# Kernel optimization log

Measured on AMD Instinct MI355X. Metric: run time of the kernel, lower is better.

The kernel has to match this reference:

```python
import jax, jax.numpy as jnp
import numpy as np

B, M = 4, 8192
NUM_PAD = 1024  # trailing pc columns zeroed to exercise the zero-column mask


def setup_inputs() -> dict:
    key = jax.random.key(0)
    k1, k2 = jax.random.split(key)
    vertices = jax.random.normal(k1, (B, 3, 128, 64), dtype=jnp.float32)
    pc = jax.random.normal(k2, (B, 3, M), dtype=jnp.float32)
    # zero-pad some columns: the original filters columns where all 3 coords == 0
    pc = pc.at[:, :, M - NUM_PAD:].set(0.0)
    return {"vertices": vertices, "pc": pc}


def reference(vertices, pc):
    b = vertices.shape[0]
    v = vertices.reshape(b, 3, -1).transpose(0, 2, 1)   # [B, N, 3] mesh vertices
    p = pc.transpose(0, 2, 1)                           # [B, M, 3] point cloud
    valid = ~jnp.all(pc == 0.0, axis=1)                 # [B, M] non-zero columns
    # squared pairwise distances pc -> vertices: [B, M, N]
    d2 = (
        jnp.sum(p * p, axis=-1)[:, :, None]
        + jnp.sum(v * v, axis=-1)[:, None, :]
        - 2.0 * jnp.einsum("bmd,bnd->bmn", p, v)
    )
    dist2 = jnp.min(d2, axis=-1)                        # [B, M] NN sq-dist per pc point
    valid_f = valid.astype(dist2.dtype)
    per_item = jnp.sum(dist2 * valid_f, axis=-1) / jnp.sum(valid_f, axis=-1)  # mean over valid points
    return jnp.mean(per_item)
```

## Files before the change

### kernel.cpp

```cpp
#include <hip/hip_runtime.h>

typedef float v2f __attribute__((ext_vector_type(2)));

#define MPTS 8192
#define NVERT 8192
#define TPB 256
#define PPT 8
#define BQ (TPB*PPT)
#define NCHUNK 32
#define VC (NVERT/NCHUNK)
#define VPAIRS (VC/2)

__global__ __launch_bounds__(TPB, 2) void minpart_kernel(
        const float* __restrict__ vert,
        const float* __restrict__ pc,
        float* __restrict__ partial)
{
    __shared__ float4 lvA[VPAIRS];
    __shared__ float4 lvB[VPAIRS];
    const int b = blockIdx.z, chunk = blockIdx.y;
    const int mbase = blockIdx.x * BQ;
    const int tid = threadIdx.x;

    const float* vb = vert + (size_t)b * 3 * NVERT + chunk * VC;
    if (tid < VPAIRS) {
        const v2f x = ((const v2f*)vb)[tid];
        const v2f y = ((const v2f*)(vb + NVERT))[tid];
        const v2f z = ((const v2f*)(vb + 2 * NVERT))[tid];
        const v2f w = x * x + y * y + z * z;
        lvA[tid] = make_float4(x.x, x.y, y.x, y.y);
        lvB[tid] = make_float4(z.x, z.y, w.x, w.y);
    }

    const float* pcb = pc + (size_t)b * 3 * MPTS;
    v2f npx[PPT], npy[PPT], npz[PPT], acc[PPT];
    #pragma unroll
    for (int p = 0; p < PPT; ++p) {
        const int m = mbase + p * TPB + tid;
        const float x = pcb[m], y = pcb[MPTS + m], z = pcb[2 * MPTS + m];
        npx[p] = (v2f){-2.0f * x, -2.0f * x};
        npy[p] = (v2f){-2.0f * y, -2.0f * y};
        npz[p] = (v2f){-2.0f * z, -2.0f * z};
        acc[p] = (v2f){1e30f, 1e30f};
    }
    __syncthreads();

    #pragma unroll 2
    for (int j = 0; j < VPAIRS; ++j) {
        const float4 A = lvA[j], Bv = lvB[j];
        const v2f vx = {A.x, A.y}, vy = {A.z, A.w};
        const v2f vz = {Bv.x, Bv.y}, vw = {Bv.z, Bv.w};
        #pragma unroll
        for (int p = 0; p < PPT; ++p) {
            const v2f t = __builtin_elementwise_fma(npx[p], vx,
                           __builtin_elementwise_fma(npy[p], vy,
                            __builtin_elementwise_fma(npz[p], vz, vw)));
            acc[p] = __builtin_elementwise_min(acc[p], t);
        }
    }

    float* po = partial + ((size_t)b * NCHUNK + chunk) * MPTS + mbase + tid;
    #pragma unroll
    for (int p = 0; p < PPT; ++p)
        po[p * TPB] = fminf(acc[p].x, acc[p].y);
}

__global__ __launch_bounds__(64) void reduce_kernel(
        const float* __restrict__ pc,
        const float* __restrict__ partial,
        v2f* __restrict__ part)
{
    const int b = blockIdx.x >> 5, sl = blockIdx.x & 31;
    const int tid = threadIdx.x;
    const int m = sl * 256 + tid * 4;
    const float* pcb = pc + (size_t)b * 3 * MPTS;
    const float* pb  = partial + (size_t)b * NCHUNK * MPTS;

    float4 t = *(const float4*)(pb + m);
    #pragma unroll 8
    for (int c = 1; c < NCHUNK; ++c) {
        const float4 u = *(const float4*)(pb + (size_t)c * MPTS + m);
        t.x = fminf(t.x, u.x); t.y = fminf(t.y, u.y);
        t.z = fminf(t.z, u.z); t.w = fminf(t.w, u.w);
    }
    const float4 x = *(const float4*)(pcb + m);
    const float4 y = *(const float4*)(pcb + MPTS + m);
    const float4 z = *(const float4*)(pcb + 2 * MPTS + m);

    float sum = 0.0f, cnt = 0.0f;
    {
        const float xs[4] = {x.x, x.y, x.z, x.w};
        const float ys[4] = {y.x, y.y, y.z, y.w};
        const float zs[4] = {z.x, z.y, z.z, z.w};
        const float ts[4] = {t.x, t.y, t.z, t.w};
        #pragma unroll
        for (int i = 0; i < 4; ++i) {
            const float d2 = fmaf(xs[i], xs[i], fmaf(ys[i], ys[i],
                             fmaf(zs[i], zs[i], ts[i])));
            if (!(xs[i] == 0.0f && ys[i] == 0.0f && zs[i] == 0.0f)) {
                sum += d2; cnt += 1.0f;
            }
        }
    }
    #pragma unroll
    for (int off = 32; off; off >>= 1) {
        sum += __shfl_down(sum, off);
        cnt += __shfl_down(cnt, off);
    }
    if (tid == 0) part[blockIdx.x] = (v2f){sum, cnt};
}

__global__ __launch_bounds__(128) void final_kernel(
        const v2f* __restrict__ part, float* __restrict__ out, int B)
{
    __shared__ float ss[128], sc[128];
    const int t = threadIdx.x;
    v2f p = (v2f){0.0f, 0.0f};
    if (t < B * 32) p = part[t];
    ss[t] = p.x; sc[t] = p.y;
    __syncthreads();
    if (t == 0) {
        float acc = 0.0f;
        for (int b = 0; b < B; ++b) {
            float s = 0.0f, c = 0.0f;
            for (int i = 0; i < 32; ++i) { s += ss[b * 32 + i]; c += sc[b * 32 + i]; }
            acc += s / c;
        }
        out[0] = acc / (float)B;
    }
}

extern "C" void kernel_launch(void* const* d_in, const int* in_sizes, int n_in,
                              void* d_out, int out_size, void* d_ws, size_t ws_size,
                              hipStream_t stream) {
    const float* vert = (const float*)d_in[0];
    const float* pc   = (const float*)d_in[1];
    float* out        = (float*)d_out;
    const int B = in_sizes[0] / (3 * NVERT);

    float* partial = (float*)d_ws;
    v2f* part = (v2f*)(partial + (size_t)B * NCHUNK * MPTS);

    dim3 grid(MPTS / BQ, NCHUNK, B);
    minpart_kernel<<<grid, TPB, 0, stream>>>(vert, pc, partial);
    reduce_kernel<<<B * 32, 64, 0, stream>>>(pc, partial, part);
    final_kernel<<<1, 128, 0, stream>>>(part, out, B);
}
```

Baseline: 83.56 us.

## Compute distance tiles with bf16x3 split MFMA instead of FP32 FMA loops

Moves the inner pairwise-distance computation onto 32x32x16 bf16 MFMA instructions. Each float operand is split into high and low bf16 parts so the dot product, plus the |v|^2 term, keeps near-FP32 accuracy. A new prep kernel packs vertex fragments into an MFMA-ready layout, and the vertex-chunk split drops from 32 to 2, which shrinks the partial-min traffic. The risks are reduced precision in the minimum distance from the truncated bf16 split and the added cost of an extra prep launch.

```diff
diff --git a/kernel.cpp b/kernel.cpp
--- a/kernel.cpp
+++ b/kernel.cpp
@@ -1,68 +1,108 @@
 #include <hip/hip_runtime.h>
 
-typedef float v2f __attribute__((ext_vector_type(2)));
+typedef float v2f    __attribute__((ext_vector_type(2)));
+typedef float f32x16 __attribute__((ext_vector_type(16)));
+typedef short short8 __attribute__((ext_vector_type(8)));
 
 #define MPTS 8192
 #define NVERT 8192
+#define NTILE (NVERT/32)
+#define NCHUNK 2
 #define TPB 256
-#define PPT 8
-#define BQ (TPB*PPT)
-#define NCHUNK 32
-#define VC (NVERT/NCHUNK)
-#define VPAIRS (VC/2)
+
+static __device__ __forceinline__ unsigned short bhi(float f) {
+    return (unsigned short)(__float_as_uint(f) >> 16);
+}
+static __device__ __forceinline__ float bf2f(unsigned short h) {
+    return __uint_as_float(((unsigned int)h) << 16);
+}
+
+__global__ __launch_bounds__(TPB) void prep_kernel(
+        const float* __restrict__ vert,
+        unsigned short* __restrict__ bfrag)
+{
+    const int idx = blockIdx.x * TPB + threadIdx.x;
+    const int b = idx >> 13, v = idx & (NVERT - 1);
+    const float* vb = vert + (size_t)b * 3 * NVERT;
+    const float x = vb[v], y = vb[v + NVERT], z = vb[v + 2 * NVERT];
+    const unsigned short hx = bhi(x), hy = bhi(y), hz = bhi(z);
+    const unsigned short lx = bhi(x - bf2f(hx));
+    const unsigned short ly = bhi(y - bf2f(hy));
+    const unsigned short lz = bhi(z - bf2f(hz));
+    const float w = fmaf(x, x, fmaf(y, y, z * z));
+    const unsigned short hw = bhi(w);
+    const unsigned short lw = bhi(w - bf2f(hw));
+
+    const int tile = v >> 5, c = v & 31;
+    unsigned short* base = bfrag + ((size_t)b * NTILE + tile) * 512;
+    short8 g0 = {(short)hx, (short)hy, (short)hz,
+                 (short)hx, (short)hy, (short)hz, (short)lx, (short)ly};
+    short8 g1 = {(short)lz, (short)hw, (short)lw, 0, 0, 0, 0, 0};
+    *(short8*)(base + c * 8)        = g0;
+    *(short8*)(base + (c + 32) * 8) = g1;
+}
 
 __global__ __launch_bounds__(TPB, 2) void minpart_kernel(
-        const float* __restrict__ vert,
+        const unsigned short* __restrict__ bfrag,
         const float* __restrict__ pc,
         float* __restrict__ partial)
 {
-    __shared__ float4 lvA[VPAIRS];
-    __shared__ float4 lvB[VPAIRS];
     const int b = blockIdx.z, chunk = blockIdx.y;
-    const int mbase = blockIdx.x * BQ;
     const int tid = threadIdx.x;
+    const int wave = tid >> 6, l = tid & 63;
+    const int half = l >> 5, lm = l & 31;
+    const int strip = blockIdx.x * 4 + wave;
+    const int pm = strip * 32 + lm;
 
-    const float* vb = vert + (size_t)b * 3 * NVERT + chunk * VC;
-    if (tid < VPAIRS) {
-        const v2f x = ((const v2f*)vb)[tid];
-        const v2f y = ((const v2f*)(vb + NVERT))[tid];
-        const v2f z = ((const v2f*)(vb + 2 * NVERT))[tid];
-        const v2f w = x * x + y * y + z * z;
-        lvA[tid] = make_float4(x.x, x.y, y.x, y.y);
-        lvB[tid] = make_float4(z.x, z.y, w.x, w.y);
+    const float* pcb = pc + (size_t)b * 3 * MPTS;
+    const float ax = -2.0f * pcb[pm];
+    const float ay = -2.0f * pcb[pm + MPTS];
+    const float az = -2.0f * pcb[pm + 2 * MPTS];
+    const unsigned short hx = bhi(ax), hy = bhi(ay), hz = bhi(az);
+    const unsigned short lx = bhi(ax - bf2f(hx));
+    const unsigned short ly = bhi(ay - bf2f(hy));
+    const unsigned short lz = bhi(az - bf2f(hz));
+    const unsigned short ONE = 0x3F80;
+
+    short8 A;
+    A[0] = half ? (short)hz : (short)hx;
+    A[1] = half ? (short)ONE : (short)hy;
+    A[2] = half ? (short)ONE : (short)hz;
+    A[3] = half ? (short)0   : (short)lx;
+    A[4] = half ? (short)0   : (short)ly;
+    A[5] = half ? (short)0   : (short)lz;
+    A[6] = half ? (short)0   : (short)hx;
+    A[7] = half ? (short)0   : (short)hy;
+
+    const unsigned short* bp =
+        bfrag + ((size_t)b * NTILE + chunk * (NTILE / NCHUNK)) * 512 + l * 8;
+
+    f32x16 run;
+    #pragma unroll
+    for (int i = 0; i < 16; ++i) run[i] = 1e30f;
+    const f32x16 zero = {};
+
+    #pragma unroll 4
+    for (int j = 0; j < NTILE / NCHUNK; ++j) {
+        const short8 bv = *(const short8*)(bp + (size_t)j * 512);
+        const f32x16 d = __builtin_amdgcn_mfma_f32_32x32x16_bf16(A, bv, zero, 0, 0, 0);
+        #pragma unroll
+        for (int i = 0; i < 16; ++i) run[i] = fminf(run[i], d[i]);
     }
 
-    const float* pcb = pc + (size_t)b * 3 * MPTS;
-    v2f npx[PPT], npy[PPT], npz[PPT], acc[PPT];
     #pragma unroll
-    for (int p = 0; p < PPT; ++p) {
-        const int m = mbase + p * TPB + tid;
-        const float x = pcb[m], y = pcb[MPTS + m], z = pcb[2 * MPTS + m];
-        npx[p] = (v2f){-2.0f * x, -2.0f * x};
-        npy[p] = (v2f){-2.0f * y, -2.0f * y};
-        npz[p] = (v2f){-2.0f * z, -2.0f * z};
-        acc[p] = (v2f){1e30f, 1e30f};
-    }
-    __syncthreads();
-
-    #pragma unroll 2
-    for (int j = 0; j < VPAIRS; ++j) {
-        const float4 A = lvA[j], Bv = lvB[j];
-        const v2f vx = {A.x, A.y}, vy = {A.z, A.w};
-        const v2f vz = {Bv.x, Bv.y}, vw = {Bv.z, Bv.w};
+    for (int m = 16; m; m >>= 1) {
         #pragma unroll
-        for (int p = 0; p < PPT; ++p) {
-            const v2f t = __builtin_elementwise_fma(npx[p], vx,
-                           __builtin_elementwise_fma(npy[p], vy,
-                            __builtin_elementwise_fma(npz[p], vz, vw)));
-            acc[p] = __builtin_elementwise_min(acc[p], t);
-        }
+        for (int i = 0; i < 16; ++i)
+            run[i] = fminf(run[i], __shfl_xor(run[i], m));
     }
 
-    float* po = partial + ((size_t)b * NCHUNK + chunk) * MPTS + mbase + tid;
-    #pragma unroll
-    for (int p = 0; p < PPT; ++p)
-        po[p * TPB] = fminf(acc[p].x, acc[p].y);
+    if (lm == 0) {
+        float* po = partial + ((size_t)b * NCHUNK + chunk) * MPTS + strip * 32;
+        #pragma unroll
+        for (int r = 0; r < 16; ++r)
+            po[(r & 3) + 8 * (r >> 2) + 4 * half] = run[r];
+    }
 }
 
 __global__ __launch_bounds__(64) void reduce_kernel(
@@ -77,7 +117,7 @@
     const float* pb  = partial + (size_t)b * NCHUNK * MPTS;
 
     float4 t = *(const float4*)(pb + m);
-    #pragma unroll 8
+    #pragma unroll
     for (int c = 1; c < NCHUNK; ++c) {
         const float4 u = *(const float4*)(pb + (size_t)c * MPTS + m);
         t.x = fminf(t.x, u.x); t.y = fminf(t.y, u.y);
@@ -138,11 +178,13 @@
     float* out        = (float*)d_out;
     const int B = in_sizes[0] / (3 * NVERT);
 
-    float* partial = (float*)d_ws;
+    unsigned short* bfrag = (unsigned short*)d_ws;
+    float* partial = (float*)((char*)d_ws + (size_t)B * NTILE * 512 * sizeof(unsigned short));
     v2f* part = (v2f*)(partial + (size_t)B * NCHUNK * MPTS);
 
-    dim3 grid(MPTS / BQ, NCHUNK, B);
-    minpart_kernel<<<grid, TPB, 0, stream>>>(vert, pc, partial);
+    prep_kernel<<<B * NVERT / TPB, TPB, 0, stream>>>(vert, bfrag);
+    dim3 grid(NVERT / 32 / 4, NCHUNK, B);
+    minpart_kernel<<<grid, TPB, 0, stream>>>(bfrag, pc, partial);
     reduce_kernel<<<B * 32, 64, 0, stream>>>(pc, partial, part);
     final_kernel<<<1, 128, 0, stream>>>(part, out, B);
 }
```

Result: no change. 84.25 us (+0.8%).
